# Optimization experiments

Hardware: AMD Instinct MI355X
Metric: run time of the kernel (lower is better)

Reference implementation:

```python
import jax, jax.numpy as jnp
import numpy as np

B, T, F, U, OUT_STEPS = 512, 48, 2048, 2048, 24


def setup_inputs() -> dict:
    key = jax.random.key(0)
    ks = jax.random.split(key, 4)
    s = 0.02  # small init scale keeps gates in a sane range
    return {
        "inputs": jax.random.normal(ks[0], (B, T, F), jnp.float32),
        "kernel": jax.random.normal(ks[1], (F, 4 * U), jnp.float32) * s,
        "rec_kernel": jax.random.normal(ks[2], (U, 4 * U), jnp.float32) * s,
        "bias": jnp.zeros((4 * U,), jnp.float32),
        "dense_w": jax.random.normal(ks[3], (U, F), jnp.float32) * s,
        "dense_b": jnp.zeros((F,), jnp.float32),
    }


def _lstm_step(h, c, x, kernel, rec_kernel, bias):
    # Keras LSTMCell: gate order i, f, c(g), o; sigmoid recurrent act, tanh act
    z = x @ kernel + h @ rec_kernel + bias  # [B, 4U]
    i, f, g, o = jnp.split(z, 4, axis=-1)
    c = jax.nn.sigmoid(f) * c + jax.nn.sigmoid(i) * jnp.tanh(g)
    h = jax.nn.sigmoid(o) * jnp.tanh(c)
    return h, c


def reference(inputs, kernel, rec_kernel, bias, dense_w, dense_b):
    Bsz = inputs.shape[0]
    Uh = rec_kernel.shape[0]
    h0 = jnp.zeros((Bsz, Uh), inputs.dtype)

    # warmup: run LSTM over the input window, keep final state
    def warm(carry, x_t):
        h, c = carry
        h, c = _lstm_step(h, c, x_t, kernel, rec_kernel, bias)
        return (h, c), None

    (h, c), _ = jax.lax.scan(warm, (h0, h0), jnp.swapaxes(inputs, 0, 1))
    pred0 = h @ dense_w + dense_b  # [B, F]

    def dec(carry, _):
        h, c, pred = carry
        h, c = _lstm_step(h, c, pred, kernel, rec_kernel, bias)
        pred = h @ dense_w + dense_b
        return (h, c, pred), pred

    _, preds = jax.lax.scan(dec, (h, c, pred0), None, length=OUT_STEPS - 1)
    preds = jnp.concatenate([pred0[None], preds], axis=0)  # [OUT, B, F]
    return jnp.transpose(preds, (1, 0, 2))  # [B, OUT, F]
```

## Files before the change

### kernel.cpp

```cpp
#include <hip/hip_runtime.h>
#include <hip/hip_bf16.h>
#include <cstddef>
#include <cstdint>

typedef __attribute__((ext_vector_type(8))) short short8;
typedef __attribute__((ext_vector_type(4))) float f32x4;
typedef unsigned short u16;
typedef unsigned int u32;

#define B_ 512
#define T_ 48
#define F_ 2048
#define U_ 2048
#define G4 8192
#define OT 24

__device__ __forceinline__ u16 f2bf(float f) {
    __hip_bfloat16 b = __float2bfloat16(f);
    return *reinterpret_cast<u16*>(&b);
}
__device__ __forceinline__ float bf2f(u16 v) {
    union { u32 u; float f; } c;
    c.u = ((u32)v) << 16;
    return c.f;
}

__device__ __forceinline__ void gl_lds16(const void* g, void* l) {
    __builtin_amdgcn_global_load_lds(
        (const __attribute__((address_space(1))) void*)g,
        (__attribute__((address_space(3))) void*)l, 16, 0, 0);
}

__device__ __forceinline__ void map_tile(int BM, int BN, int& m0, int& n0) {
    const int gx = gridDim.x, gy = gridDim.y;
    int lin = blockIdx.y * gx + blockIdx.x;
    const int nwg = gx * gy;
    const int sn = gx >> 3;
    const int EN = (sn >= 4) ? 4 : sn;
    const int EM = 4;
    bool ok = ((gx & 7) == 0) && ((gy & 3) == 0) && (sn < 4 || (sn & 3) == 0);
    if (ok) {
        int xcd = lin & 7, idx = lin >> 3;
        int epw = EM * EN;
        int e = idx / epw, r = idx % epw;
        int meb = gy / EM;
        int ne = e / meb, me = e % meb;
        int mi = r % EM, nli = r / EM;
        int m = me * EM + mi;
        int nl = ne * EN + nli;
        m0 = m * BM;
        n0 = (xcd * sn + nl) * BN;
    } else {
        if ((nwg & 7) == 0) {
            int q = nwg >> 3;
            lin = (lin & 7) * q + (lin >> 3);
        }
        m0 = (lin / gx) * BM;
        n0 = (lin % gx) * BN;
    }
}

template <int ILV>
__global__ void transpose_f32_bf16(const float* __restrict__ in,
                                   u16* __restrict__ out, int R, int C) {
    __shared__ float tile[32][33];
    int bx = blockIdx.x * 32;
    int by = blockIdx.y * 32;
    int tx = threadIdx.x, ty = threadIdx.y;
#pragma unroll
    for (int j = 0; j < 32; j += 8)
        tile[ty + j][tx] = in[(size_t)(by + ty + j) * C + bx + tx];
    __syncthreads();
#pragma unroll
    for (int j = 0; j < 32; j += 8) {
        int cidx = bx + ty + j;
        int orow = ILV ? (((cidx & 2047) << 2) | (cidx >> 11)) : cidx;
        out[(size_t)orow * R + by + tx] = f2bf(tile[tx][ty + j]);
    }
}

__global__ void cvt_bf16(const float* __restrict__ in, u16* __restrict__ out, long n) {
    long i = ((long)blockIdx.x * blockDim.x + threadIdx.x) * 4;
    if (i >= n) return;
    f32x4 v = *(const f32x4*)(in + i);
    ushort4 o;
    o.x = f2bf(v[0]); o.y = f2bf(v[1]); o.z = f2bf(v[2]); o.w = f2bf(v[3]);
    *(ushort4*)(out + i) = o;
}

__global__ void cvt_x_tmajor(const float* __restrict__ x, u16* __restrict__ xbf) {
    long i = ((long)blockIdx.x * blockDim.x + threadIdx.x) * 4;
    int f = (int)(i & (F_ - 1));
    long bt = i >> 11;
    int t = (int)(bt % T_);
    int b = (int)(bt / T_);
    f32x4 v = *(const f32x4*)(x + i);
    ushort4 o;
    o.x = f2bf(v[0]); o.y = f2bf(v[1]); o.z = f2bf(v[2]); o.w = f2bf(v[3]);
    *(ushort4*)(xbf + ((size_t)t * B_ + b) * F_ + f) = o;
}

__global__ void make_bias4(const float* __restrict__ bias, float* __restrict__ b4) {
    int n = blockIdx.x * 256 + threadIdx.x;
    int g = n & 3, u = n >> 2;
    b4[n] = bias[g * 2048 + u];
}

__global__ void bcomb_k(const u16* __restrict__ W4kT, const float* __restrict__ bd,
                        const float* __restrict__ bias4, float* __restrict__ bc) {
    int lane = threadIdx.x & 63, wid = threadIdx.x >> 6;
    int n = blockIdx.x * 4 + wid;
    const u16* row = W4kT + (size_t)n * U_;
    float s = 0.f;
    for (int j0 = lane * 8; j0 < U_; j0 += 512) {
        short8 v = *(const short8*)&row[j0];
#pragma unroll
        for (int e = 0; e < 8; ++e) s += bd[j0 + e] * bf2f((u16)v[e]);
    }
#pragma unroll
    for (int o = 32; o; o >>= 1) s += __shfl_down(s, o);
    if (lane == 0) bc[n] = bias4[n] + s;
}

template <int BM, int BN, int BK>
__device__ __forceinline__ void gpass(const u16* __restrict__ A, long lda,
                                      const u16* __restrict__ B, int K,
                                      int m0, int n0, int tid,
                                      u16* As, u16* Bs,
                                      f32x4 (&acc)[BM / 32][BN / 32]) {
    const int lane = tid & 63, wid = tid >> 6;
    const int wr = wid >> 1, wc = wid & 1;
    const int r16 = lane & 15, kg = lane >> 4;
    constexpr int MF = BM / 32, NF = BN / 32;
    constexpr int S = BK / 8;
    constexpr int RPI = 64 / S;
    constexpr int AIS = BM / RPI / 4;
    constexpr int BIS = BN / RPI / 4;
    constexpr int ABUF = BM * BK, BBUF = BN * BK;
    const int rl = lane / S;
    const int sl = lane % S;
    const int sw = (sl ^ (rl & (S - 1))) * 8;

    auto stage = [&](int kt, int buf) {
#pragma unroll
        for (int i = 0; i < AIS; ++i) {
            int chunk = wid * AIS + i;
            gl_lds16(A + (size_t)(m0 + chunk * RPI + rl) * lda + kt + sw,
                     As + buf * ABUF + chunk * RPI * BK);
        }
#pragma unroll
        for (int i = 0; i < BIS; ++i) {
            int chunk = wid * BIS + i;
            gl_lds16(B + (size_t)(n0 + chunk * RPI + rl) * (size_t)K + kt + sw,
                     Bs + buf * BBUF + chunk * RPI * BK);
        }
    };
    auto compute = [&](int buf) {
        __builtin_amdgcn_s_setprio(1);
#pragma unroll
        for (int ks = 0; ks < BK / 32; ++ks) {
            short8 af[MF], bfv[NF];
#pragma unroll
            for (int mi = 0; mi < MF; ++mi) {
                int row = wr * (BM / 2) + mi * 16 + r16;
                int s = (ks * 4 + kg) ^ (row & (S - 1));
                af[mi] = *(const short8*)&As[buf * ABUF + row * BK + s * 8];
            }
#pragma unroll
            for (int ni = 0; ni < NF; ++ni) {
                int row = wc * (BN / 2) + ni * 16 + r16;
                int s = (ks * 4 + kg) ^ (row & (S - 1));
                bfv[ni] = *(const short8*)&Bs[buf * BBUF + row * BK + s * 8];
            }
#pragma unroll
            for (int mi = 0; mi < MF; ++mi)
#pragma unroll
                for (int ni = 0; ni < NF; ++ni)
                    acc[mi][ni] = __builtin_amdgcn_mfma_f32_16x16x32_bf16(
                        af[mi], bfv[ni], acc[mi][ni], 0, 0, 0);
        }
        __builtin_amdgcn_s_setprio(0);
    };

    __syncthreads();
    stage(0, 0);
    __syncthreads();
    int cur = 0;
    for (int kt = BK; kt < K; kt += BK) {
        stage(kt, cur ^ 1);
        compute(cur);
        __syncthreads();
        cur ^= 1;
    }
    compute(cur);
}

template <int BM, int BN, int CM, int HAS2, int BIAS, int OUTM>
__global__ __launch_bounds__(256) void gemm2(
    const u16* __restrict__ A1, long lda1, const u16* __restrict__ B1, int K1,
    const u16* __restrict__ A2, long lda2, const u16* __restrict__ B2, int K2,
    const void* __restrict__ Ci, long ldci, const float* __restrict__ bias,
    void* __restrict__ Co, long ldc, void* __restrict__ Co2, long ldc2) {
    __shared__ __align__(16) u16 As[2 * BM * 32];
    __shared__ __align__(16) u16 Bs[2 * BN * 32];
    int m0, n0;
    map_tile(BM, BN, m0, n0);
    const int tid = threadIdx.x;

    f32x4 acc[BM / 32][BN / 32] = {};
    gpass<BM, BN, 32>(A1, lda1, B1, K1, m0, n0, tid, As, Bs, acc);
    if constexpr (HAS2) gpass<BM, BN, 32>(A2, lda2, B2, K2, m0, n0, tid, As, Bs, acc);

    const int lane = tid & 63, wid = tid >> 6;
    const int wr = wid >> 1, wc = wid & 1, r16 = lane & 15, rg = lane >> 4;
#pragma unroll
    for (int ni = 0; ni < BN / 32; ++ni) {
        int col = n0 + wc * (BN / 2) + ni * 16 + r16;
        float bv = BIAS ? bias[col] : 0.f;
#pragma unroll
        for (int mi = 0; mi < BM / 32; ++mi) {
#pragma unroll
            for (int r = 0; r < 4; ++r) {
                int row = m0 + wr * (BM / 2) + mi * 16 + rg * 4 + r;
                float v = acc[mi][ni][r] + bv;
                if constexpr (CM == 1) v += ((const float*)Ci)[(size_t)row * ldci + col];
                if constexpr (CM == 2) v += bf2f(((const u16*)Ci)[(size_t)row * ldci + col]);
                if constexpr (OUTM == 0) ((float*)Co)[(size_t)row * ldc + col] = v;
                if constexpr (OUTM == 1) ((u16*)Co)[(size_t)row * ldc + col] = f2bf(v);
                if constexpr (OUTM == 2) {
                    int t = row >> 9, b = row & 511;
                    ((float*)Co)[((size_t)b * OT + t) * F_ + col] = v;
                }
                if constexpr (OUTM == 3) {
                    ((float*)Co)[(size_t)row * ldc + col] = v;
                    ((u16*)Co2)[(size_t)row * ldc2 + col] = f2bf(v);
                }
            }
        }
    }
}

template <int WARM>
__global__ __launch_bounds__(256) void lstm_step(
    const u16* __restrict__ A1, long lda1, const u16* __restrict__ B1,
    const u16* __restrict__ A2, long lda2, const u16* __restrict__ B2,
    const u16* __restrict__ zx, const float* __restrict__ bc4,
    float* __restrict__ c, u16* __restrict__ hout) {
    constexpr int BM = 64, BN = 128, BK = 64;
    __shared__ __align__(16) char smem[49152];
    u16* As = (u16*)smem;
    u16* Bs = (u16*)(smem + 2 * BM * BK * 2);
    float* zt = (float*)smem;

    int m0, n0;
    map_tile(BM, BN, m0, n0);
    const int tid = threadIdx.x;

    f32x4 acc[2][4] = {};
    gpass<BM, BN, BK>(A1, lda1, B1, U_, m0, n0, tid, As, Bs, acc);
    if constexpr (WARM == 2) gpass<BM, BN, BK>(A2, lda2, B2, U_, m0, n0, tid, As, Bs, acc);

    __syncthreads();
    {
        const int lane = tid & 63, wid = tid >> 6;
        const int wr = wid >> 1, wc = wid & 1, r16 = lane & 15, rg = lane >> 4;
#pragma unroll
        for (int mi = 0; mi < 2; ++mi)
#pragma unroll
            for (int ni = 0; ni < 4; ++ni)
#pragma unroll
                for (int r = 0; r < 4; ++r)
                    zt[(wr * 32 + mi * 16 + rg * 4 + r) * 132 + wc * 64 + ni * 16 + r16] =
                        acc[mi][ni][r];
    }
    __syncthreads();

    const int row = tid >> 5, ul = tid & 31;
    const int ug = (n0 >> 2) + ul;
#pragma unroll
    for (int j = 0; j < 8; ++j) {
        int rr = j * 8 + row;
        f32x4 zv = *(const f32x4*)&zt[rr * 132 + 4 * ul];
        float zi = zv[0], zf = zv[1], zg = zv[2], zo = zv[3];
        if constexpr (WARM == 1) {
            ushort4 zb = *(const ushort4*)&zx[(size_t)(m0 + rr) * G4 + n0 + 4 * ul];
            zi += bf2f(zb.x); zf += bf2f(zb.y); zg += bf2f(zb.z); zo += bf2f(zb.w);
        } else {
            f32x4 bv = *(const f32x4*)&bc4[n0 + 4 * ul];
            zi += bv[0]; zf += bv[1]; zg += bv[2]; zo += bv[3];
        }
        size_t ci = (size_t)(m0 + rr) * U_ + ug;
        float si = 1.f / (1.f + __expf(-zi));
        float sf = 1.f / (1.f + __expf(-zf));
        float so = 1.f / (1.f + __expf(-zo));
        float cc = sf * c[ci] + si * tanhf(zg);
        c[ci] = cc;
        hout[ci] = f2bf(so * tanhf(cc));
    }
}

extern "C" void kernel_launch(void* const* d_in, const int* in_sizes, int n_in,
                              void* d_out, int out_size, void* d_ws, size_t ws_size,
                              hipStream_t stream) {
    const float* x = (const float*)d_in[0];
    const float* Wk = (const float*)d_in[1];
    const float* Wr = (const float*)d_in[2];
    const float* bias = (const float*)d_in[3];
    const float* Wd = (const float*)d_in[4];
    const float* bd = (const float*)d_in[5];
    float* out = (float*)d_out;

    u16* xbf = (u16*)d_out;

    auto pad = [](size_t s) { return (s + 255) & ~(size_t)255; };
    const size_t szW4 = (size_t)G4 * U_ * 2;
    const size_t szDT = (size_t)U_ * F_ * 2;
    const size_t szB4 = (size_t)G4 * 4;
    const size_t szH = (size_t)OT * B_ * U_ * 2;
    const size_t szHP = (size_t)B_ * U_ * 2;
    const size_t szC = (size_t)B_ * U_ * 4;
    const size_t szZX1 = (size_t)B_ * G4 * 2;
    const size_t SLOT = (size_t)B_ * U_;

    const size_t needMain = pad(szW4) * 3 + pad(szDT) * 2 + pad(szB4) * 2 +
                            pad(szH) + pad(szHP) * 2 + pad(szC) + pad(szZX1);
    const int path = ws_size >= needMain ? 1 : 0;

    char* p = (char*)d_ws;
    auto alloc = [&](size_t bytes) { void* r = p; p += (bytes + 255) & ~(size_t)255; return r; };

    dim3 tb32(32, 8);
    const dim3 gstep(64, 8);

    if (path == 1) {
        u16* W4kT = (u16*)alloc(szW4);
        u16* W4rT = (u16*)alloc(szW4);
        u16* W4cT = (u16*)alloc(szW4);
        u16* dT = (u16*)alloc(szDT);
        u16* dbf = (u16*)alloc(szDT);
        float* bias4 = (float*)alloc(szB4);
        float* bc4 = (float*)alloc(szB4);
        u16* H = (u16*)alloc(szH);
        u16* hp0 = (u16*)alloc(szHP);
        u16* hp1 = (u16*)alloc(szHP);
        float* c = (float*)alloc(szC);

        size_t avail = ws_size - (size_t)(p - (char*)d_ws);
        int chunk = (int)(avail / szZX1);
        if (chunk > T_) chunk = T_;
        u16* ZX = (u16*)alloc((size_t)chunk * szZX1);

        cvt_x_tmajor<<<(B_ * T_ * F_ / 4 + 255) / 256, 256, 0, stream>>>(x, xbf);
        transpose_f32_bf16<1><<<dim3(G4 / 32, F_ / 32), tb32, 0, stream>>>(Wk, W4kT, F_, G4);
        transpose_f32_bf16<1><<<dim3(G4 / 32, U_ / 32), tb32, 0, stream>>>(Wr, W4rT, U_, G4);
        transpose_f32_bf16<0><<<dim3(F_ / 32, U_ / 32), tb32, 0, stream>>>(Wd, dT, U_, F_);
        cvt_bf16<<<(U_ * F_ / 4 + 255) / 256, 256, 0, stream>>>(Wd, dbf, (long)U_ * F_);
        make_bias4<<<G4 / 256, 256, 0, stream>>>(bias, bias4);
        bcomb_k<<<G4 / 4, 256, 0, stream>>>(W4kT, bd, bias4, bc4);

        gemm2<128, 128, 2, 0, 0, 1><<<dim3(U_ / 128, G4 / 128), 256, 0, stream>>>(
            W4kT, U_, dbf, F_, nullptr, 0, nullptr, 0, W4rT, U_, nullptr,
            W4cT, U_, nullptr, 0);

        hipMemsetAsync(c, 0, szC, stream);
        hipMemsetAsync(hp0, 0, szHP, stream);

        for (int t0 = 0; t0 < T_; t0 += chunk) {
            int nc = chunk < T_ - t0 ? chunk : T_ - t0;
            gemm2<128, 128, 0, 0, 1, 1><<<dim3(G4 / 128, nc * B_ / 128), 256, 0, stream>>>(
                xbf + (size_t)t0 * B_ * F_, F_, W4kT, F_, nullptr, 0, nullptr, 0,
                nullptr, 0, bias4, ZX, G4, nullptr, 0);
            for (int t = t0; t < t0 + nc; ++t) {
                const u16* hin = (t & 1) ? hp1 : hp0;
                u16* hout = (t == T_ - 1) ? H : ((t & 1) ? hp0 : hp1);
                lstm_step<1><<<gstep, 256, 0, stream>>>(
                    hin, U_, W4rT, nullptr, 0, nullptr,
                    ZX + (size_t)(t - t0) * B_ * G4, nullptr, c, hout);
            }
        }
        for (int t = 1; t < OT; ++t) {
            lstm_step<0><<<gstep, 256, 0, stream>>>(
                H + (size_t)(t - 1) * SLOT, U_, W4cT, nullptr, 0, nullptr,
                nullptr, bc4, c, H + (size_t)t * SLOT);
        }
        gemm2<128, 128, 0, 0, 1, 2><<<dim3(F_ / 128, OT * B_ / 128), 256, 0, stream>>>(
            H, U_, dT, U_, nullptr, 0, nullptr, 0, nullptr, 0, bd, out, F_, nullptr, 0);
    } else {
        u16* W4kT = (u16*)alloc(szW4);
        u16* W4rT = (u16*)alloc(szW4);
        u16* dT = (u16*)alloc(szDT);
        float* bias4 = (float*)alloc(szB4);
        u16* hp0 = (u16*)alloc(szHP);
        u16* hp1 = (u16*)alloc(szHP);
        u16* pred = (u16*)alloc(szHP);
        float* c = (float*)alloc(szC);

        cvt_x_tmajor<<<(B_ * T_ * F_ / 4 + 255) / 256, 256, 0, stream>>>(x, xbf);
        transpose_f32_bf16<1><<<dim3(G4 / 32, F_ / 32), tb32, 0, stream>>>(Wk, W4kT, F_, G4);
        transpose_f32_bf16<1><<<dim3(G4 / 32, U_ / 32), tb32, 0, stream>>>(Wr, W4rT, U_, G4);
        transpose_f32_bf16<0><<<dim3(F_ / 32, U_ / 32), tb32, 0, stream>>>(Wd, dT, U_, F_);
        make_bias4<<<G4 / 256, 256, 0, stream>>>(bias, bias4);
        hipMemsetAsync(c, 0, szC, stream);
        hipMemsetAsync(hp0, 0, szHP, stream);

        u16* hin = hp0;
        u16* hout = hp1;
        for (int t = 0; t < T_; ++t) {
            lstm_step<2><<<gstep, 256, 0, stream>>>(
                hin, U_, W4rT, xbf + (size_t)t * B_ * F_, F_, W4kT,
                nullptr, bias4, c, hout);
            u16* tmp = hin; hin = hout; hout = tmp;
        }
        gemm2<64, 128, 0, 0, 1, 3><<<dim3(F_ / 128, B_ / 64), 256, 0, stream>>>(
            hin, U_, dT, U_, nullptr, 0, nullptr, 0, nullptr, 0, bd,
            out, (long)OT * F_, pred, U_);
        for (int t = 1; t < OT; ++t) {
            lstm_step<2><<<gstep, 256, 0, stream>>>(
                hin, U_, W4rT, pred, U_, W4kT, nullptr, bias4, c, hout);
            u16* tmp = hin; hin = hout; hout = tmp;
            gemm2<64, 128, 0, 0, 1, 3><<<dim3(F_ / 128, B_ / 64), 256, 0, stream>>>(
                hin, U_, dT, U_, nullptr, 0, nullptr, 0, nullptr, 0, bd,
                out + (size_t)t * F_, (long)OT * F_, pred, U_);
        }
    }
}
```

Measured before the change: 3.238 ms.

## Replace double-buffered GEMM mainloop with triple-buffered vmcnt pipeline and larger tiles

Replaces the two-stage LDS pipeline, which synchronised on every K step, with a three-stage ring buffer at BK=64. Partial s_waitcnt vmcnt counts let global-to-LDS loads for the next two tiles overlap MFMA compute. The large GEMMs (weight combine, input projection, final dense) move to 256x128 tiles with 512 threads and 8 waves. The per-step LSTM kernels use the new pipeline. This raises LDS use per block and depends on hand-written vmcnt literals that assume exactly 6 loads per stage.

```diff
diff --git a/kernel.cpp b/kernel.cpp
--- a/kernel.cpp
+++ b/kernel.cpp
@@ -46,10 +46,8 @@
         int meb = gy / EM;
         int ne = e / meb, me = e % meb;
         int mi = r % EM, nli = r / EM;
-        int m = me * EM + mi;
-        int nl = ne * EN + nli;
-        m0 = m * BM;
-        n0 = (xcd * sn + nl) * BN;
+        m0 = (me * EM + mi) * BM;
+        n0 = (xcd * sn + ne * EN + nli) * BN;
     } else {
         if ((nwg & 7) == 0) {
             int q = nwg >> 3;
@@ -122,108 +120,110 @@
     if (lane == 0) bc[n] = bias4[n] + s;
 }
 
-template <int BM, int BN, int BK>
-__device__ __forceinline__ void gpass(const u16* __restrict__ A, long lda,
+template <int BM, int BN, int WR, int WC, int TPB>
+__device__ __forceinline__ void gpipe(const u16* __restrict__ A, long lda,
                                       const u16* __restrict__ B, int K,
-                                      int m0, int n0, int tid,
-                                      u16* As, u16* Bs,
-                                      f32x4 (&acc)[BM / 32][BN / 32]) {
+                                      int m0, int n0, int tid, u16* lds,
+                                      f32x4 (&acc)[BM / WR / 16][BN / WC / 16]) {
+    constexpr int BK = 64;
+    constexpr int MF = BM / WR / 16, NF = BN / WC / 16;
+    constexpr int TILE = (BM + BN) * BK;
+    constexpr int LA = BM * BK / (TPB * 8);
+    constexpr int LB = BN * BK / (TPB * 8);
+    static_assert(LA + LB == 6, "vmcnt literals assume 6 loads per stage");
     const int lane = tid & 63, wid = tid >> 6;
-    const int wr = wid >> 1, wc = wid & 1;
+    const int wr = wid / WC, wc = wid % WC;
     const int r16 = lane & 15, kg = lane >> 4;
-    constexpr int MF = BM / 32, NF = BN / 32;
-    constexpr int S = BK / 8;
-    constexpr int RPI = 64 / S;
-    constexpr int AIS = BM / RPI / 4;
-    constexpr int BIS = BN / RPI / 4;
-    constexpr int ABUF = BM * BK, BBUF = BN * BK;
-    const int rl = lane / S;
-    const int sl = lane % S;
-    const int sw = (sl ^ (rl & (S - 1))) * 8;
-
-    auto stage = [&](int kt, int buf) {
-#pragma unroll
-        for (int i = 0; i < AIS; ++i) {
-            int chunk = wid * AIS + i;
-            gl_lds16(A + (size_t)(m0 + chunk * RPI + rl) * lda + kt + sw,
-                     As + buf * ABUF + chunk * RPI * BK);
-        }
-#pragma unroll
-        for (int i = 0; i < BIS; ++i) {
-            int chunk = wid * BIS + i;
-            gl_lds16(B + (size_t)(n0 + chunk * RPI + rl) * (size_t)K + kt + sw,
-                     Bs + buf * BBUF + chunk * RPI * BK);
+    const int NT = K / BK;
+
+    auto stage = [&](int t) {
+        if (t >= NT) return;
+        const u16* Abase = A + (size_t)m0 * lda + (size_t)t * BK;
+        const u16* Bbase = B + (size_t)n0 * (size_t)K + (size_t)t * BK;
+        u16* dst = lds + (t % 3) * TILE;
+#pragma unroll
+        for (int i = 0; i < LA; ++i) {
+            int idx = i * TPB + tid;
+            int r = idx >> 3, sl = idx & 7;
+            gl_lds16(Abase + (size_t)r * lda + ((sl ^ (r & 7)) * 8), dst + idx * 8);
+        }
+        u16* dstB = dst + BM * BK;
+#pragma unroll
+        for (int i = 0; i < LB; ++i) {
+            int idx = i * TPB + tid;
+            int r = idx >> 3, sl = idx & 7;
+            gl_lds16(Bbase + (size_t)r * (size_t)K + ((sl ^ (r & 7)) * 8), dstB + idx * 8);
         }
     };
-    auto compute = [&](int buf) {
+    auto compute = [&](int t) {
+        const u16* Ab = lds + (t % 3) * TILE;
+        const u16* Bb = Ab + BM * BK;
         __builtin_amdgcn_s_setprio(1);
 #pragma unroll
-        for (int ks = 0; ks < BK / 32; ++ks) {
-            short8 af[MF], bfv[NF];
+        for (int ks = 0; ks < 2; ++ks) {
+            short8 af[MF], bf[NF];
 #pragma unroll
             for (int mi = 0; mi < MF; ++mi) {
-                int row = wr * (BM / 2) + mi * 16 + r16;
-                int s = (ks * 4 + kg) ^ (row & (S - 1));
-                af[mi] = *(const short8*)&As[buf * ABUF + row * BK + s * 8];
+                int row = wr * (BM / WR) + mi * 16 + r16;
+                int s = (ks * 4 + kg) ^ (row & 7);
+                af[mi] = *(const short8*)&Ab[row * BK + s * 8];
             }
 #pragma unroll
             for (int ni = 0; ni < NF; ++ni) {
-                int row = wc * (BN / 2) + ni * 16 + r16;
-                int s = (ks * 4 + kg) ^ (row & (S - 1));
-                bfv[ni] = *(const short8*)&Bs[buf * BBUF + row * BK + s * 8];
+                int row = wc * (BN / WC) + ni * 16 + r16;
+                int s = (ks * 4 + kg) ^ (row & 7);
+                bf[ni] = *(const short8*)&Bb[row * BK + s * 8];
             }
 #pragma unroll
             for (int mi = 0; mi < MF; ++mi)
 #pragma unroll
                 for (int ni = 0; ni < NF; ++ni)
                     acc[mi][ni] = __builtin_amdgcn_mfma_f32_16x16x32_bf16(
-                        af[mi], bfv[ni], acc[mi][ni], 0, 0, 0);
+                        af[mi], bf[ni], acc[mi][ni], 0, 0, 0);
         }
         __builtin_amdgcn_s_setprio(0);
     };
 
-    __syncthreads();
-    stage(0, 0);
-    __syncthreads();
-    int cur = 0;
-    for (int kt = BK; kt < K; kt += BK) {
-        stage(kt, cur ^ 1);
-        compute(cur);
-        __syncthreads();
-        cur ^= 1;
-    }
-    compute(cur);
-}
-
-template <int BM, int BN, int CM, int HAS2, int BIAS, int OUTM>
-__global__ __launch_bounds__(256) void gemm2(
+    stage(0);
+    stage(1);
+    for (int t = 0; t < NT; ++t) {
+        stage(t + 2);
+        if (t + 2 < NT)
+            asm volatile("s_waitcnt vmcnt(12)\ns_barrier" ::: "memory");
+        else if (t + 1 < NT)
+            asm volatile("s_waitcnt vmcnt(6)\ns_barrier" ::: "memory");
+        else
+            asm volatile("s_waitcnt vmcnt(0)\ns_barrier" ::: "memory");
+        compute(t);
+        asm volatile("s_barrier" ::: "memory");
+    }
+}
+
+template <int BM, int BN, int WR, int WC, int TPB, int CM, int BIAS, int OUTM>
+__global__ __launch_bounds__(TPB) void gemm3(
     const u16* __restrict__ A1, long lda1, const u16* __restrict__ B1, int K1,
-    const u16* __restrict__ A2, long lda2, const u16* __restrict__ B2, int K2,
     const void* __restrict__ Ci, long ldci, const float* __restrict__ bias,
     void* __restrict__ Co, long ldc, void* __restrict__ Co2, long ldc2) {
-    __shared__ __align__(16) u16 As[2 * BM * 32];
-    __shared__ __align__(16) u16 Bs[2 * BN * 32];
+    __shared__ __align__(16) u16 lds[3 * (BM + BN) * 64];
     int m0, n0;
     map_tile(BM, BN, m0, n0);
     const int tid = threadIdx.x;
 
-    f32x4 acc[BM / 32][BN / 32] = {};
-    gpass<BM, BN, 32>(A1, lda1, B1, K1, m0, n0, tid, As, Bs, acc);
-    if constexpr (HAS2) gpass<BM, BN, 32>(A2, lda2, B2, K2, m0, n0, tid, As, Bs, acc);
+    f32x4 acc[BM / WR / 16][BN / WC / 16] = {};
+    gpipe<BM, BN, WR, WC, TPB>(A1, lda1, B1, K1, m0, n0, tid, lds, acc);
 
     const int lane = tid & 63, wid = tid >> 6;
-    const int wr = wid >> 1, wc = wid & 1, r16 = lane & 15, rg = lane >> 4;
-#pragma unroll
-    for (int ni = 0; ni < BN / 32; ++ni) {
-        int col = n0 + wc * (BN / 2) + ni * 16 + r16;
+    const int wr = wid / WC, wc = wid % WC, r16 = lane & 15, rg = lane >> 4;
+#pragma unroll
+    for (int ni = 0; ni < BN / WC / 16; ++ni) {
+        int col = n0 + wc * (BN / WC) + ni * 16 + r16;
         float bv = BIAS ? bias[col] : 0.f;
 #pragma unroll
-        for (int mi = 0; mi < BM / 32; ++mi) {
+        for (int mi = 0; mi < BM / WR / 16; ++mi) {
 #pragma unroll
             for (int r = 0; r < 4; ++r) {
-                int row = m0 + wr * (BM / 2) + mi * 16 + rg * 4 + r;
+                int row = m0 + wr * (BM / WR) + mi * 16 + rg * 4 + r;
                 float v = acc[mi][ni][r] + bv;
-                if constexpr (CM == 1) v += ((const float*)Ci)[(size_t)row * ldci + col];
                 if constexpr (CM == 2) v += bf2f(((const u16*)Ci)[(size_t)row * ldci + col]);
                 if constexpr (OUTM == 0) ((float*)Co)[(size_t)row * ldc + col] = v;
                 if constexpr (OUTM == 1) ((u16*)Co)[(size_t)row * ldc + col] = f2bf(v);
@@ -246,10 +246,9 @@
     const u16* __restrict__ A2, long lda2, const u16* __restrict__ B2,
     const u16* __restrict__ zx, const float* __restrict__ bc4,
     float* __restrict__ c, u16* __restrict__ hout) {
-    constexpr int BM = 64, BN = 128, BK = 64;
-    __shared__ __align__(16) char smem[49152];
-    u16* As = (u16*)smem;
-    u16* Bs = (u16*)(smem + 2 * BM * BK * 2);
+    constexpr int BM = 64, BN = 128;
+    __shared__ __align__(16) char smem[3 * (BM + BN) * 64 * 2];
+    u16* lds = (u16*)smem;
     float* zt = (float*)smem;
 
     int m0, n0;
@@ -257,8 +256,9 @@
     const int tid = threadIdx.x;
 
     f32x4 acc[2][4] = {};
-    gpass<BM, BN, BK>(A1, lda1, B1, U_, m0, n0, tid, As, Bs, acc);
-    if constexpr (WARM == 2) gpass<BM, BN, BK>(A2, lda2, B2, U_, m0, n0, tid, As, Bs, acc);
+    gpipe<BM, BN, 2, 2, 256>(A1, lda1, B1, U_, m0, n0, tid, lds, acc);
+    if constexpr (WARM == 2)
+        gpipe<BM, BN, 2, 2, 256>(A2, lda2, B2, U_, m0, n0, tid, lds, acc);
 
     __syncthreads();
     {
@@ -358,18 +358,25 @@
         make_bias4<<<G4 / 256, 256, 0, stream>>>(bias, bias4);
         bcomb_k<<<G4 / 4, 256, 0, stream>>>(W4kT, bd, bias4, bc4);
 
-        gemm2<128, 128, 2, 0, 0, 1><<<dim3(U_ / 128, G4 / 128), 256, 0, stream>>>(
-            W4kT, U_, dbf, F_, nullptr, 0, nullptr, 0, W4rT, U_, nullptr,
-            W4cT, U_, nullptr, 0);
+        gemm3<256, 128, 4, 2, 512, 2, 0, 1><<<dim3(U_ / 128, G4 / 256), 512, 0, stream>>>(
+            W4kT, U_, dbf, F_, W4rT, U_, nullptr, W4cT, U_, nullptr, 0);
 
         hipMemsetAsync(c, 0, szC, stream);
         hipMemsetAsync(hp0, 0, szHP, stream);
 
         for (int t0 = 0; t0 < T_; t0 += chunk) {
             int nc = chunk < T_ - t0 ? chunk : T_ - t0;
-            gemm2<128, 128, 0, 0, 1, 1><<<dim3(G4 / 128, nc * B_ / 128), 256, 0, stream>>>(
-                xbf + (size_t)t0 * B_ * F_, F_, W4kT, F_, nullptr, 0, nullptr, 0,
-                nullptr, 0, bias4, ZX, G4, nullptr, 0);
+            if ((nc * B_) % 256 == 0) {
+                gemm3<256, 128, 4, 2, 512, 0, 1, 1>
+                    <<<dim3(G4 / 128, nc * B_ / 256), 512, 0, stream>>>(
+                        xbf + (size_t)t0 * B_ * F_, F_, W4kT, F_, nullptr, 0,
+                        bias4, ZX, G4, nullptr, 0);
+            } else {
+                gemm3<64, 128, 2, 2, 256, 0, 1, 1>
+                    <<<dim3(G4 / 128, nc * B_ / 64), 256, 0, stream>>>(
+                        xbf + (size_t)t0 * B_ * F_, F_, W4kT, F_, nullptr, 0,
+                        bias4, ZX, G4, nullptr, 0);
+            }
             for (int t = t0; t < t0 + nc; ++t) {
                 const u16* hin = (t & 1) ? hp1 : hp0;
                 u16* hout = (t == T_ - 1) ? H : ((t & 1) ? hp0 : hp1);
@@ -383,8 +390,8 @@
                 H + (size_t)(t - 1) * SLOT, U_, W4cT, nullptr, 0, nullptr,
                 nullptr, bc4, c, H + (size_t)t * SLOT);
         }
-        gemm2<128, 128, 0, 0, 1, 2><<<dim3(F_ / 128, OT * B_ / 128), 256, 0, stream>>>(
-            H, U_, dT, U_, nullptr, 0, nullptr, 0, nullptr, 0, bd, out, F_, nullptr, 0);
+        gemm3<256, 128, 4, 2, 512, 0, 1, 2><<<dim3(F_ / 128, OT * B_ / 256), 512, 0, stream>>>(
+            H, U_, dT, U_, nullptr, 0, bd, out, F_, nullptr, 0);
     } else {
         u16* W4kT = (u16*)alloc(szW4);
         u16* W4rT = (u16*)alloc(szW4);
@@ -411,16 +418,14 @@
                 nullptr, bias4, c, hout);
             u16* tmp = hin; hin = hout; hout = tmp;
         }
-        gemm2<64, 128, 0, 0, 1, 3><<<dim3(F_ / 128, B_ / 64), 256, 0, stream>>>(
-            hin, U_, dT, U_, nullptr, 0, nullptr, 0, nullptr, 0, bd,
-            out, (long)OT * F_, pred, U_);
+        gemm3<64, 128, 2, 2, 256, 0, 1, 3><<<dim3(F_ / 128, B_ / 64), 256, 0, stream>>>(
+            hin, U_, dT, U_, nullptr, 0, bd, out, (long)OT * F_, pred, U_);
         for (int t = 1; t < OT; ++t) {
             lstm_step<2><<<gstep, 256, 0, stream>>>(
                 hin, U_, W4rT, pred, U_, W4kT, nullptr, bias4, c, hout);
             u16* tmp = hin; hin = hout; hout = tmp;
-            gemm2<64, 128, 0, 0, 1, 3><<<dim3(F_ / 128, B_ / 64), 256, 0, stream>>>(
-                hin, U_, dT, U_, nullptr, 0, nullptr, 0, nullptr, 0, bd,
-                out + (size_t)t * F_, (long)OT * F_, pred, U_);
-        }
-    }
-}
+            gemm3<64, 128, 2, 2, 256, 0, 1, 3><<<dim3(F_ / 128, B_ / 64), 256, 0, stream>>>(
+                hin, U_, dT, U_, nullptr, 0, bd, out + (size_t)t * F_, (long)OT * F_, pred, U_);
+        }
+    }
+}
```

Result: no change. 3.235 ms (-0.1%).
